# Kernel tuning notes

Measured on AMD Instinct MI355X. Metric: run time of the kernel, lower is better.

Reference implementation:

```python
import jax, jax.numpy as jnp
import numpy as np

N_NODES = 100000
N_EDGES = 1600000
N_GRAPHS = 1000
HID = 128
NCLS = 3


def setup_inputs() -> dict:
    key = jax.random.key(0)
    ks = jax.random.split(key, 16)
    x = jax.random.normal(ks[0], (N_NODES, 1), dtype=jnp.float32)
    edge_index = jax.random.randint(ks[1], (2, N_EDGES), 0, N_NODES, dtype=jnp.int64)
    edge_attr = jax.random.normal(ks[2], (N_EDGES, 1), dtype=jnp.float32)
    batch = jnp.sort(jax.random.randint(ks[3], (N_NODES,), 0, N_GRAPHS, dtype=jnp.int64))
    s1 = 1.0 / np.sqrt(1.0)
    sh = 1.0 / np.sqrt(HID)
    # layer 0 MLP: 1 -> HID -> HID
    W1_0 = jax.random.uniform(ks[4], (1, HID), minval=-s1, maxval=s1)
    b1_0 = jax.random.uniform(ks[5], (HID,), minval=-s1, maxval=s1)
    W2_0 = jax.random.uniform(ks[6], (HID, HID), minval=-sh, maxval=sh)
    b2_0 = jax.random.uniform(ks[7], (HID,), minval=-sh, maxval=sh)
    # layers 1..3 MLPs stacked: HID -> HID -> HID
    W1_s = jax.random.uniform(ks[8], (3, HID, HID), minval=-sh, maxval=sh)
    b1_s = jax.random.uniform(ks[9], (3, HID), minval=-sh, maxval=sh)
    W2_s = jax.random.uniform(ks[10], (3, HID, HID), minval=-sh, maxval=sh)
    b2_s = jax.random.uniform(ks[11], (3, HID), minval=-sh, maxval=sh)
    Wc = jax.random.uniform(ks[12], (HID, NCLS), minval=-sh, maxval=sh)
    bc = jax.random.uniform(ks[13], (NCLS,), minval=-sh, maxval=sh)
    return {"x": x, "edge_index": edge_index, "edge_attr": edge_attr, "batch": batch,
            "W1_0": W1_0, "b1_0": b1_0, "W2_0": W2_0, "b2_0": b2_0,
            "W1_s": W1_s, "b1_s": b1_s, "W2_s": W2_s, "b2_s": b2_s,
            "Wc": Wc, "bc": bc}


def _gine_layer(x, src, dst, edge_attr, W1, b1, W2, b2):
    # message: ReLU(x_j + e_ji), broadcast over feature dim ([E,1] edge_attr)
    msg = jax.nn.relu(x[src] + edge_attr)                       # [E, F]
    agg = jax.ops.segment_sum(msg, dst, num_segments=x.shape[0])  # [N, F]
    h = x + agg                                                 # (1 + eps)*x + agg, eps = 0
    return jax.nn.relu(h @ W1 + b1) @ W2 + b2                   # MLP


def reference(x, edge_index, edge_attr, batch,
              W1_0, b1_0, W2_0, b2_0, W1_s, b1_s, W2_s, b2_s, Wc, bc):
    src, dst = edge_index[0], edge_index[1]
    h = jax.nn.relu(_gine_layer(x, src, dst, edge_attr, W1_0, b1_0, W2_0, b2_0))
    for i in range(3):
        h = jax.nn.relu(_gine_layer(h, src, dst, edge_attr,
                                    W1_s[i], b1_s[i], W2_s[i], b2_s[i]))
    # global mean pool per graph
    summed = jax.ops.segment_sum(h, batch, num_segments=N_GRAPHS)       # [G, HID]
    counts = jax.ops.segment_sum(jnp.ones((h.shape[0],), h.dtype), batch,
                                 num_segments=N_GRAPHS)                  # [G]
    pooled = summed / jnp.maximum(counts, 1.0)[:, None]
    return pooled @ Wc + bc                                              # [G, NCLS]
```

## Files before the change

### kernel.cpp

```cpp
#include <hip/hip_runtime.h>
#include <hip/hip_bf16.h>


#define HID 128
#define NCLS 3
#define EPB 8192
#define BSHIFT 6
#define BNODES 64
#define ECAP 2040

typedef _Float16 f16;
typedef f16 f16x2 __attribute__((ext_vector_type(2)));
typedef f16 f16x8 __attribute__((ext_vector_type(8)));
typedef float f32x2 __attribute__((ext_vector_type(2)));
typedef float f32x4 __attribute__((ext_vector_type(4)));
typedef unsigned short ushort;

__device__ __forceinline__ float bcf(int v) {
    return __builtin_bit_cast(float, v);
}
__device__ __forceinline__ float f16bits2f(ushort u) {
    return (float)__builtin_bit_cast(f16, u);
}


__global__ __launch_bounds__(1024) void k_bin2(const int* __restrict__ src,
                                               const int* __restrict__ dst,
                                               const float* __restrict__ eattr,
                                               const float* __restrict__ x,
                                               int* __restrict__ cursor,
                                               int2* __restrict__ ebuf,
                                               int E, int NB) {
    __shared__ int lh[2048];
    __shared__ int lbase[2048];
    __shared__ int lrsv[2048];
    int t = threadIdx.x;
    for (int b = t; b < NB; b += 1024) lh[b] = 0;
    __syncthreads();
    int base = blockIdx.x * EPB;
    int myd[8];
    #pragma unroll
    for (int j = 0; j < 8; ++j) {
        int e = base + j * 1024 + t;
        myd[j] = (e < E) ? dst[e] : -1;
        if (myd[j] >= 0) atomicAdd(&lh[myd[j] >> BSHIFT], 1);
    }
    __syncthreads();
    for (int b = t; b < NB; b += 1024) {
        int c = lh[b];
        int cp = (c + 7) & ~7;
        lrsv[b] = cp;
        lbase[b] = (cp > 0) ? (b * ECAP + atomicAdd(&cursor[b], cp)) : 0;
        lh[b] = 0;
    }
    __syncthreads();
    #pragma unroll
    for (int j = 0; j < 8; ++j) {
        if (myd[j] >= 0) {
            int e = base + j * 1024 + t;
            int b = myd[j] >> BSHIFT;
            int s = src[e];
            float at = eattr[e];
            float msg = fmaxf(x[s] + at, 0.f);
            unsigned a16 = __builtin_bit_cast(ushort, (f16)at);
            unsigned m16 = __builtin_bit_cast(ushort, (f16)msg);
            int r = atomicAdd(&lh[b], 1);
            int pos = lbase[b] + r;
            if (pos < (b + 1) * ECAP)
                ebuf[pos] = make_int2(s | ((myd[j] & (BNODES - 1)) << 24),
                                      (int)((a16 << 16) | m16));
        }
    }
    __syncthreads();
    for (int b = t; b < NB; b += 1024) {
        int c = lh[b], cp = lrsv[b];
        int p0 = lbase[b] + c;
        int pe = lbase[b] + cp;
        int cap = (b + 1) * ECAP;
        if (pe > cap) pe = cap;
        for (int pos = p0; pos < pe; ++pos)
            ebuf[pos] = make_int2(-1, 0);
    }
}


__global__ __launch_bounds__(1024) void k_prep(const float* __restrict__ W2_0,
                                               const float* __restrict__ W1_s,
                                               const float* __restrict__ W2_s,
                                               f16* __restrict__ Wf,
                                               const int* __restrict__ cursor,
                                               int* __restrict__ bbase, int NB) {
    int t = threadIdx.x;
    if (blockIdx.x < 14) {
        int id = blockIdx.x * 1024 + t;
        int lane = id & 63;
        int w    = (id >> 6) & 3;
        int nf   = (id >> 8) & 1;
        int kk   = (id >> 9) & 3;
        int g    = id >> 11;
        const float* W = (g == 0) ? W2_0
                       : ((g & 1) ? W1_s + (size_t)((g - 1) >> 1) * HID * HID
                                  : W2_s + (size_t)((g - 2) >> 1) * HID * HID);
        int col = w * 32 + nf * 16 + (lane & 15);
        int k0  = kk * 32 + (lane >> 4) * 8;
        f16x8 hi;
        #pragma unroll
        for (int j = 0; j < 8; ++j)
            hi[j] = (f16)W[(k0 + j) * HID + col];
        size_t o = ((((size_t)g * 4 + kk) * 2 + nf) * 4 + w) * 512 +
                   (size_t)lane * 8;
        *(f16x8*)&Wf[o] = hi;
    } else {
        __shared__ int sd[1024];
        int i0 = 2 * t, i1 = 2 * t + 1;
        int a = (i0 < NB) ? min(cursor[i0], ECAP) : 0;
        int b = (i1 < NB) ? min(cursor[i1], ECAP) : 0;
        int s = a + b;
        sd[t] = s;
        __syncthreads();
        #pragma unroll
        for (int o = 1; o < 1024; o <<= 1) {
            int add = (t >= o) ? sd[t - o] : 0;
            __syncthreads();
            sd[t] += add;
            __syncthreads();
        }
        int excl = sd[t] - s;
        if (i0 < NB) bbase[i0] = excl;
        if (i1 < NB) bbase[i1] = excl + a;
        if (t == 1023) bbase[NB] = sd[1023];
    }
}

__global__ __launch_bounds__(256, 8) void k_fill2(const int2* __restrict__ ebuf,
                                               const int* __restrict__ btot,
                                               const int* __restrict__ bbase,
                                               const float* __restrict__ x,
                                               const int* __restrict__ batch,
                                               int2* __restrict__ meta,
                                               int2* __restrict__ pairs,
                                               float* __restrict__ hin0,
                                               int* __restrict__ gcount,
                                               int* __restrict__ gstart,
                                               int N) {
    __shared__ int lcnt[BNODES];
    __shared__ int lofs[BNODES];
    __shared__ float satom[BNODES];
    int b = blockIdx.x, t = threadIdx.x;
    int estart = b * ECAP;
    int cnt = min(btot[b], ECAP);
    int pstart = bbase[b];
    int nb0 = b << BSHIFT;
    if (t < BNODES) {
        lcnt[t] = 0;
        satom[t] = 0.f;
        int node = nb0 + t;
        if (node < N) {
            int gb = batch[node];
            atomicAdd(&gcount[gb], 1);
            if (node == 0 || batch[node - 1] != gb) gstart[gb] = node;
        }
    }
    __syncthreads();
    int2 myv[8];
    #pragma unroll
    for (int j = 0; j < 8; ++j) {
        int i = j * 256 + t;
        if (i < cnt) myv[j] = ebuf[estart + i];
    }
    #pragma unroll
    for (int j = 0; j < 8; ++j) {
        int i = j * 256 + t;
        if (i < cnt && myv[j].x != -1)
            atomicAdd(&lcnt[((unsigned)myv[j].x) >> 24], 1);
    }
    __syncthreads();
    if (t < 64) {
        int a = lcnt[t];
        int sa = a;
        #pragma unroll
        for (int o = 1; o < 64; o <<= 1) {
            int v = __shfl_up(sa, o);
            if (t >= o) sa += v;
        }
        int ea = sa - a;
        lofs[t] = ea;
        lcnt[t] = 0;
        int n0 = nb0 + t;
        if (n0 < N) meta[n0] = make_int2(pstart + ea, a);
    }
    __syncthreads();
    #pragma unroll
    for (int j = 0; j < 8; ++j) {
        int i = j * 256 + t;
        if (i < cnt) {
            int2 v = myv[j];
            if (v.x != -1) {
                int ld = ((unsigned)v.x) >> 24;
                int srcid = v.x & 0x00FFFFFF;
                ushort a16 = (ushort)(((unsigned)v.y) >> 16);
                ushort m16 = (ushort)(v.y & 0xFFFF);
                int r = atomicAdd(&lcnt[ld], 1);
                int pos = lofs[ld] + r;
                pairs[pstart + pos] = make_int2(srcid << 7,
                                     __builtin_bit_cast(int, f16bits2f(a16)));
                atomicAdd(&satom[ld], f16bits2f(m16));
            }
        }
    }
    __syncthreads();
    if (t < BNODES) {
        int node = nb0 + t;
        if (node < N) hin0[node] = x[node] + satom[t];
    }
}


__device__ __forceinline__ void agg_add8(f32x2 acc2[4], uint2 g, float e) {
    f32x2 e2 = {e, e}, z2 = {0.f, 0.f};
    unsigned gw[2] = {g.x, g.y};
    #pragma unroll
    for (int ww = 0; ww < 2; ++ww) {
        f32x2 lo = __builtin_amdgcn_cvt_pk_f32_fp8((int)gw[ww], false);
        f32x2 hi = __builtin_amdgcn_cvt_pk_f32_fp8((int)gw[ww], true);
        lo = __builtin_elementwise_max(lo + e2, z2);
        hi = __builtin_elementwise_max(hi + e2, z2);
        acc2[2 * ww]     += lo;
        acc2[2 * ww + 1] += hi;
    }
}

__device__ __forceinline__ uint2 agg_ld8(const char* __restrict__ hb,
                                         int voff) {
    return *(const uint2*)(hb + (unsigned)voff);
}

__global__ __launch_bounds__(256, 4) void k_agg(
    const unsigned char* __restrict__ h8,
    const f16* __restrict__ hf,
    const int2* __restrict__ pairs,
    const int2* __restrict__ meta,
    f16* __restrict__ oh, int n) {

    int t = threadIdx.x;
    int w = t >> 6, lane = t & 63;
    int g = lane >> 4, c = lane & 15;
    int node = blockIdx.x * 16 + w * 4 + g;
    int c8 = c * 8;
    int sbase = g * 16;
    const char* hb = (const char*)h8;

    int2 m = make_int2(0, 0);
    if (node < n) m = meta[node];
    int off = m.x, d = m.y;
    f32x2 acc2[4] = {{0.f,0.f},{0.f,0.f},{0.f,0.f},{0.f,0.f}};

    for (int wb = 0; wb < d; wb += 16) {
        int rem = d - wb;
        int mm = rem < 16 ? rem : 16;
        int2 pr = make_int2(0, 0);
        if (c < mm) pr = pairs[off + wb + c];
        uint2 gg[16];
        #pragma unroll
        for (int p = 0; p < 16; ++p) {
            int s = __shfl(pr.x, sbase + p);
            if (p < mm) gg[p] = agg_ld8(hb, s + c8);
        }
        #pragma unroll
        for (int p = 0; p < 16; ++p) {
            if (p < mm) {
                float e = bcf(__shfl(pr.y, sbase + p));
                agg_add8(acc2, gg[p], e);
            }
        }
    }

    if (node < n) {
        uint4 sg = *(const uint4*)&hf[(size_t)node * HID + c8];
        unsigned sw[4] = {sg.x, sg.y, sg.z, sg.w};
        unsigned ow[4];
        #pragma unroll
        for (int ww = 0; ww < 4; ++ww) {
            f16x2 s = __builtin_bit_cast(f16x2, sw[ww]);
            f16x2 o;
            o[0] = (f16)((float)s[0] + acc2[ww].x);
            o[1] = (f16)((float)s[1] + acc2[ww].y);
            ow[ww] = __builtin_bit_cast(unsigned, o);
        }
        uint4 o4;
        o4.x = ow[0]; o4.y = ow[1]; o4.z = ow[2]; o4.w = ow[3];
        *(uint4*)&oh[(size_t)node * HID + c8] = o4;
    }
}


__device__ __forceinline__ void load_wfrags1(const f16* __restrict__ Wfg,
                                             int w, int lane,
                                             f16x8 whf[4][2]) {
    #pragma unroll
    for (int kk = 0; kk < 4; ++kk)
        #pragma unroll
        for (int nf = 0; nf < 2; ++nf) {
            size_t o = (((size_t)kk * 2 + nf) * 4 + w) * 512 +
                       (size_t)lane * 8;
            whf[kk][nf] = *(const f16x8*)&Wfg[o];
        }
}

__device__ __forceinline__ void do_gemm1(const f16* Ah,
                                         const f16x8 whf[4][2],
                                         int lane, f32x4 acc[4][2]) {
    int arow = lane & 15, akgrp = lane >> 4;
    #pragma unroll
    for (int kk = 0; kk < 4; ++kk) {
        int chunk = kk * 4 + akgrp;
        f16x8 ah[4];
        #pragma unroll
        for (int mf = 0; mf < 4; ++mf) {
            int r = mf * 16 + arow;
            int swz = chunk ^ (r & 15);
            ah[mf] = *(const f16x8*)&Ah[r * HID + swz * 8];
        }
        #pragma unroll
        for (int mf = 0; mf < 4; ++mf)
            #pragma unroll
            for (int nf = 0; nf < 2; ++nf)
                acc[mf][nf] = __builtin_amdgcn_mfma_f32_16x16x32_f16(
                    ah[mf], whf[kk][nf], acc[mf][nf], 0, 0, 0);
    }
}


__global__ __launch_bounds__(256, 3) void k_mlp(
    const f16* __restrict__ A_g,
    const f16* __restrict__ Wf1, const float* __restrict__ b1,
    const f16* __restrict__ Wf2, const float* __restrict__ b2,
    f16* __restrict__ O, unsigned char* __restrict__ O8, int w8, int n) {

    __shared__ __align__(16) f16 bufA[64 * HID];
    int t = threadIdx.x, w = t >> 6, lane = t & 63;
    int wcol = w * 32, fcol = lane & 15, kgrp = lane >> 4;
    int row0 = blockIdx.x * 64;

    #pragma unroll
    for (int rep = 0; rep < 4; ++rep) {
        int task = rep * 256 + t;
        int r = task >> 4, ch = task & 15;
        int gr = min(row0 + r, n - 1);
        int swz = ch ^ (r & 15);
        *(f16x8*)&bufA[r * HID + swz * 8] =
            *(const f16x8*)&A_g[(size_t)gr * HID + ch * 8];
    }

    f32x4 acc[4][2];
    {
        f16x8 whf[4][2];
        load_wfrags1(Wf1, w, lane, whf);
        float bv0 = b1[wcol + fcol], bv1 = b1[wcol + 16 + fcol];
        __syncthreads();
        #pragma unroll
        for (int mf = 0; mf < 4; ++mf)
            #pragma unroll
            for (int nf = 0; nf < 2; ++nf)
                acc[mf][nf] = (f32x4)(0.f);
        do_gemm1(bufA, whf, lane, acc);
        __syncthreads();
        #pragma unroll
        for (int mf = 0; mf < 4; ++mf)
            #pragma unroll
            for (int nf = 0; nf < 2; ++nf) {
                int cc = wcol + nf * 16 + fcol;
                float bb = nf ? bv1 : bv0;
                #pragma unroll
                for (int j = 0; j < 4; ++j) {
                    int r = mf * 16 + kgrp * 4 + j;
                    float v = fmaxf(acc[mf][nf][j] + bb, 0.f);
                    int addr = r * HID + (((cc >> 3) ^ (r & 15)) << 3) + (cc & 7);
                    bufA[addr] = (f16)v;
                }
            }
    }
    {
        f16x8 whf[4][2];
        load_wfrags1(Wf2, w, lane, whf);
        float bv0 = b2[wcol + fcol], bv1 = b2[wcol + 16 + fcol];
        __syncthreads();
        #pragma unroll
        for (int mf = 0; mf < 4; ++mf)
            #pragma unroll
            for (int nf = 0; nf < 2; ++nf)
                acc[mf][nf] = (f32x4)(0.f);
        do_gemm1(bufA, whf, lane, acc);

        #pragma unroll
        for (int mf = 0; mf < 4; ++mf)
            #pragma unroll
            for (int nf = 0; nf < 2; ++nf) {
                int cc = wcol + nf * 16 + fcol;
                float bb = nf ? bv1 : bv0;
                #pragma unroll
                for (int j = 0; j < 4; ++j) {
                    int r = row0 + mf * 16 + kgrp * 4 + j;
                    if (r < n) {
                        float v = fmaxf(acc[mf][nf][j] + bb, 0.f);
                        O[(size_t)r * HID + cc] = (f16)v;
                        if (w8) {
                            int pk = __builtin_amdgcn_cvt_pk_fp8_f32(
                                v, v, 0, false);
                            O8[(size_t)r * HID + cc] =
                                (unsigned char)(pk & 0xFF);
                        }
                    }
                }
            }
    }
}


__global__ __launch_bounds__(256, 3) void k_mlp0(
    const float* __restrict__ r1x, const float* __restrict__ r1w,
    const float* __restrict__ r1b,
    const f16* __restrict__ Wf2, const float* __restrict__ b2,
    f16* __restrict__ O, unsigned char* __restrict__ O8, int n) {

    __shared__ __align__(16) f16 bufA[64 * HID];
    int t = threadIdx.x, w = t >> 6, lane = t & 63;
    int wcol = w * 32, fcol = lane & 15, kgrp = lane >> 4;
    int row0 = blockIdx.x * 64;

    #pragma unroll
    for (int rep = 0; rep < 4; ++rep) {
        int task = rep * 256 + t;
        int r = task >> 4, ch = task & 15;
        int gr = min(row0 + r, n - 1);
        int swz = ch ^ (r & 15);
        float xv = r1x[gr];
        f16x8 hi;
        #pragma unroll
        for (int j = 0; j < 8; ++j)
            hi[j] = (f16)fmaxf(xv * r1w[ch * 8 + j] + r1b[ch * 8 + j], 0.f);
        *(f16x8*)&bufA[r * HID + swz * 8] = hi;
    }

    f16x8 whf[4][2];
    load_wfrags1(Wf2, w, lane, whf);
    float bv0 = b2[wcol + fcol], bv1 = b2[wcol + 16 + fcol];
    __syncthreads();
    f32x4 acc[4][2];
    #pragma unroll
    for (int mf = 0; mf < 4; ++mf)
        #pragma unroll
        for (int nf = 0; nf < 2; ++nf)
            acc[mf][nf] = (f32x4)(0.f);
    do_gemm1(bufA, whf, lane, acc);

    #pragma unroll
    for (int mf = 0; mf < 4; ++mf)
        #pragma unroll
        for (int nf = 0; nf < 2; ++nf) {
            int cc = wcol + nf * 16 + fcol;
            float bb = nf ? bv1 : bv0;
            #pragma unroll
            for (int j = 0; j < 4; ++j) {
                int r = row0 + mf * 16 + kgrp * 4 + j;
                if (r < n) {
                    float v = fmaxf(acc[mf][nf][j] + bb, 0.f);
                    O[(size_t)r * HID + cc] = (f16)v;
                    int pk = __builtin_amdgcn_cvt_pk_fp8_f32(v, v, 0, false);
                    O8[(size_t)r * HID + cc] = (unsigned char)(pk & 0xFF);
                }
            }
        }
}


__global__ __launch_bounds__(256) void k_head(const f16* __restrict__ h,
                                              const int* __restrict__ gstart,
                                              const int* __restrict__ gcount,
                                              const float* __restrict__ Wc,
                                              const float* __restrict__ bc,
                                              float* __restrict__ out, int G) {
    __shared__ float2 red[4][64];
    __shared__ float pl[HID];
    int g = blockIdx.x, t = threadIdx.x;
    int rr = t >> 6, cc = t & 63;
    int st = gstart[g], c = gcount[g];
    float2 acc = make_float2(0.f, 0.f);
    for (int i = rr; i < c; i += 4) {
        unsigned u = *(const unsigned*)&h[(size_t)(st + i) * HID + cc * 2];
        f16x2 v = __builtin_bit_cast(f16x2, u);
        acc.x += (float)v[0];
        acc.y += (float)v[1];
    }
    red[rr][cc] = acc;
    __syncthreads();
    if (rr == 0) {
        #pragma unroll
        for (int k = 1; k < 4; ++k) {
            acc.x += red[k][cc].x;
            acc.y += red[k][cc].y;
        }
        float inv = 1.f / fmaxf((float)c, 1.f);
        pl[cc * 2]     = acc.x * inv;
        pl[cc * 2 + 1] = acc.y * inv;
    }
    __syncthreads();
    if (t < NCLS) {
        float o = bc[t];
        for (int k = 0; k < HID; ++k) o += pl[k] * Wc[k * NCLS + t];
        out[g * NCLS + t] = o;
    }
}


static inline size_t alignup(size_t x, size_t a) { return (x + a - 1) & ~(a - 1); }

extern "C" void kernel_launch(void* const* d_in, const int* in_sizes, int n_in,
                              void* d_out, int out_size, void* d_ws, size_t ws_size,
                              hipStream_t stream) {
    const float* x      = (const float*)d_in[0];
    const int*   ei     = (const int*)d_in[1];
    const float* eattr  = (const float*)d_in[2];
    const int*   batch  = (const int*)d_in[3];
    const float* W1_0   = (const float*)d_in[4];
    const float* b1_0   = (const float*)d_in[5];
    const float* W2_0   = (const float*)d_in[6];
    const float* b2_0   = (const float*)d_in[7];
    const float* W1_s   = (const float*)d_in[8];
    const float* b1_s   = (const float*)d_in[9];
    const float* W2_s   = (const float*)d_in[10];
    const float* b2_s   = (const float*)d_in[11];
    const float* Wc     = (const float*)d_in[12];
    const float* bc     = (const float*)d_in[13];

    const int N = in_sizes[0];
    const int E = in_sizes[2];
    const int G = out_size / NCLS;
    const int* srcI = ei;
    const int* dstI = ei + E;

    const int NB = (N + BNODES - 1) >> BSHIFT;
    const int NBLK = (E + EPB - 1) / EPB;

    char* p = (char*)d_ws;
    size_t off = 0;
    size_t gcount_off = off;         off = alignup(off + (size_t)G * 4, 256);
    size_t gstart_off = off;         off = alignup(off + (size_t)G * 4, 256);
    size_t cursor_off = off;         off = alignup(off + 2048 * 4, 256);
    size_t zero_bytes = off;
    size_t meta_off = off;           off = alignup(off + (size_t)N * 8, 256);
    size_t bbase_off = off;          off = alignup(off + 2049 * 4, 256);
    size_t hin0_off = off;           off = alignup(off + (size_t)N * 4, 256);
    size_t wf_off = off;             off = alignup(off + 7 * 16384 * 2, 256);
    size_t pairs_off = off;          off = alignup(off + (size_t)NB * ECAP * 8, 256);
    size_t p0_off = off;             off = alignup(off + (size_t)N * HID * 2, 256);
    size_t p8_off = off;             off = alignup(off + (size_t)N * HID, 256);
    size_t p1_off = off;             off = alignup(off + (size_t)N * HID * 2, 256);

    int*    gcount  = (int*)(p + gcount_off);
    int*    gstart  = (int*)(p + gstart_off);
    int*    cursor  = (int*)(p + cursor_off);
    int2*   meta    = (int2*)(p + meta_off);
    int*    bbase   = (int*)(p + bbase_off);
    float*  hin0    = (float*)(p + hin0_off);
    f16*    Wf      = (f16*)(p + wf_off);
    int2*   pairs   = (int2*)(p + pairs_off);
    f16*    P0      = (f16*)(p + p0_off);
    unsigned char* P8 = (unsigned char*)(p + p8_off);
    f16*    P1      = (f16*)(p + p1_off);
    int2*   ebuf    = (int2*)(p + p1_off);

    hipMemsetAsync(d_ws, 0, zero_bytes, stream);

    int gblk = (N + 63) / 64;
    int abl = (N + 15) / 16;

    k_bin2<<<NBLK, 1024, 0, stream>>>(srcI, dstI, eattr, x, cursor, ebuf,
                                      E, NB);
    k_prep<<<15, 1024, 0, stream>>>(W2_0, W1_s, W2_s, Wf, cursor, bbase, NB);
    k_fill2<<<NB, 256, 0, stream>>>(ebuf, cursor, bbase, x, batch, meta,
                                    pairs, hin0, gcount, gstart, N);

    #define WFG(g) (Wf + (size_t)(g) * 16384)

    k_mlp0<<<gblk, 256, 0, stream>>>(hin0, W1_0, b1_0, WFG(0), b2_0,
                                     P0, P8, N);

    for (int l = 0; l < 3; ++l) {
        const float* b1 = b1_s + (size_t)l * HID;
        const float* b2 = b2_s + (size_t)l * HID;
        k_agg<<<abl, 256, 0, stream>>>(P8, P0, pairs, meta, P1, N);
        k_mlp<<<gblk, 256, 0, stream>>>(P1, WFG(1 + 2 * l), b1,
                                        WFG(2 + 2 * l), b2, P0, P8,
                                        (l < 2) ? 1 : 0, N);
    }

    k_head<<<G, 256, 0, stream>>>(P0, gstart, gcount, Wc, bc,
                                  (float*)d_out, G);
}
```

Baseline: 315.4 us.

## Fuse neighbor aggregation into MLP kernel with ping-pong feature buffers

Merges the aggregation kernel into the MLP kernel. Each block now gathers and sums neighbor messages for its 64 rows straight into shared memory, so the fp16 intermediate no longer makes a round trip through global memory and three kernel launches go away. The layers now ping-pong between two fp16/fp8 buffer pairs, because a layer can no longer overwrite its own input in place. The trade-off is that the irregular gather now runs inside a kernel with lower occupancy (launch bounds 3), and its latency is exposed before the MFMA work starts.

```diff
diff --git a/kernel.cpp b/kernel.cpp
--- a/kernel.cpp
+++ b/kernel.cpp
@@ -235,64 +235,6 @@
     return *(const uint2*)(hb + (unsigned)voff);
 }
 
-__global__ __launch_bounds__(256, 4) void k_agg(
-    const unsigned char* __restrict__ h8,
-    const f16* __restrict__ hf,
-    const int2* __restrict__ pairs,
-    const int2* __restrict__ meta,
-    f16* __restrict__ oh, int n) {
-
-    int t = threadIdx.x;
-    int w = t >> 6, lane = t & 63;
-    int g = lane >> 4, c = lane & 15;
-    int node = blockIdx.x * 16 + w * 4 + g;
-    int c8 = c * 8;
-    int sbase = g * 16;
-    const char* hb = (const char*)h8;
-
-    int2 m = make_int2(0, 0);
-    if (node < n) m = meta[node];
-    int off = m.x, d = m.y;
-    f32x2 acc2[4] = {{0.f,0.f},{0.f,0.f},{0.f,0.f},{0.f,0.f}};
-
-    for (int wb = 0; wb < d; wb += 16) {
-        int rem = d - wb;
-        int mm = rem < 16 ? rem : 16;
-        int2 pr = make_int2(0, 0);
-        if (c < mm) pr = pairs[off + wb + c];
-        uint2 gg[16];
-        #pragma unroll
-        for (int p = 0; p < 16; ++p) {
-            int s = __shfl(pr.x, sbase + p);
-            if (p < mm) gg[p] = agg_ld8(hb, s + c8);
-        }
-        #pragma unroll
-        for (int p = 0; p < 16; ++p) {
-            if (p < mm) {
-                float e = bcf(__shfl(pr.y, sbase + p));
-                agg_add8(acc2, gg[p], e);
-            }
-        }
-    }
-
-    if (node < n) {
-        uint4 sg = *(const uint4*)&hf[(size_t)node * HID + c8];
-        unsigned sw[4] = {sg.x, sg.y, sg.z, sg.w};
-        unsigned ow[4];
-        #pragma unroll
-        for (int ww = 0; ww < 4; ++ww) {
-            f16x2 s = __builtin_bit_cast(f16x2, sw[ww]);
-            f16x2 o;
-            o[0] = (f16)((float)s[0] + acc2[ww].x);
-            o[1] = (f16)((float)s[1] + acc2[ww].y);
-            ow[ww] = __builtin_bit_cast(unsigned, o);
-        }
-        uint4 o4;
-        o4.x = ow[0]; o4.y = ow[1]; o4.z = ow[2]; o4.w = ow[3];
-        *(uint4*)&oh[(size_t)node * HID + c8] = o4;
-    }
-}
-
 
 __device__ __forceinline__ void load_wfrags1(const f16* __restrict__ Wfg,
                                              int w, int lane,
@@ -331,25 +273,63 @@
 }
 
 
-__global__ __launch_bounds__(256, 3) void k_mlp(
-    const f16* __restrict__ A_g,
+__global__ __launch_bounds__(256, 3) void k_aggmlp(
+    const unsigned char* __restrict__ h8, const f16* __restrict__ hf,
+    const int2* __restrict__ pairs, const int2* __restrict__ meta,
     const f16* __restrict__ Wf1, const float* __restrict__ b1,
     const f16* __restrict__ Wf2, const float* __restrict__ b2,
     f16* __restrict__ O, unsigned char* __restrict__ O8, int w8, int n) {
 
     __shared__ __align__(16) f16 bufA[64 * HID];
     int t = threadIdx.x, w = t >> 6, lane = t & 63;
-    int wcol = w * 32, fcol = lane & 15, kgrp = lane >> 4;
+    int g = lane >> 4, c = lane & 15;
+    int wcol = w * 32, fcol = c, kgrp = g;
+    int c8 = c * 8, sbase = g * 16;
     int row0 = blockIdx.x * 64;
-
-    #pragma unroll
-    for (int rep = 0; rep < 4; ++rep) {
-        int task = rep * 256 + t;
-        int r = task >> 4, ch = task & 15;
-        int gr = min(row0 + r, n - 1);
-        int swz = ch ^ (r & 15);
-        *(f16x8*)&bufA[r * HID + swz * 8] =
-            *(const f16x8*)&A_g[(size_t)gr * HID + ch * 8];
+    const char* hb = (const char*)h8;
+
+    #pragma unroll
+    for (int pass = 0; pass < 4; ++pass) {
+        int r = w * 16 + pass * 4 + g;
+        int node = row0 + r;
+        int2 m = make_int2(0, 0);
+        if (node < n) m = meta[node];
+        int off = m.x, d = m.y;
+        f32x2 acc2[4] = {{0.f,0.f},{0.f,0.f},{0.f,0.f},{0.f,0.f}};
+
+        for (int wb = 0; wb < d; wb += 16) {
+            int rem = d - wb;
+            int mm = rem < 16 ? rem : 16;
+            int2 pr = make_int2(0, 0);
+            if (c < mm) pr = pairs[off + wb + c];
+            uint2 gg[16];
+            #pragma unroll
+            for (int p = 0; p < 16; ++p) {
+                int s = __shfl(pr.x, sbase + p);
+                if (p < mm) gg[p] = agg_ld8(hb, s + c8);
+            }
+            #pragma unroll
+            for (int p = 0; p < 16; ++p) {
+                if (p < mm) {
+                    float e = bcf(__shfl(pr.y, sbase + p));
+                    agg_add8(acc2, gg[p], e);
+                }
+            }
+        }
+
+        f16x8 ov = (f16x8)(f16)0.f;
+        if (node < n) {
+            uint4 sg = *(const uint4*)&hf[(size_t)node * HID + c8];
+            unsigned sw[4] = {sg.x, sg.y, sg.z, sg.w};
+            #pragma unroll
+            for (int ww = 0; ww < 4; ++ww) {
+                f16x2 s = __builtin_bit_cast(f16x2, sw[ww]);
+                ov[2 * ww]     = (f16)((float)s[0] + acc2[ww].x);
+                ov[2 * ww + 1] = (f16)((float)s[1] + acc2[ww].y);
+            }
+        }
+        int swz = c ^ (r & 15);
+        *(f16x8*)&bufA[r * HID + swz * 8] = ov;
     }
 
     f32x4 acc[4][2];
@@ -553,9 +533,10 @@
     size_t hin0_off = off;           off = alignup(off + (size_t)N * 4, 256);
     size_t wf_off = off;             off = alignup(off + 7 * 16384 * 2, 256);
     size_t pairs_off = off;          off = alignup(off + (size_t)NB * ECAP * 8, 256);
-    size_t p0_off = off;             off = alignup(off + (size_t)N * HID * 2, 256);
-    size_t p8_off = off;             off = alignup(off + (size_t)N * HID, 256);
-    size_t p1_off = off;             off = alignup(off + (size_t)N * HID * 2, 256);
+    size_t p0f_off = off;            off = alignup(off + (size_t)N * HID * 2, 256);
+    size_t p0q_off = off;            off = alignup(off + (size_t)N * HID, 256);
+    size_t p1f_off = off;            off = alignup(off + (size_t)N * HID * 2, 256);
+    size_t p1q_off = off;            off = alignup(off + (size_t)N * HID, 256);
 
     int*    gcount  = (int*)(p + gcount_off);
     int*    gstart  = (int*)(p + gstart_off);
@@ -565,15 +546,15 @@
     float*  hin0    = (float*)(p + hin0_off);
     f16*    Wf      = (f16*)(p + wf_off);
     int2*   pairs   = (int2*)(p + pairs_off);
-    f16*    P0      = (f16*)(p + p0_off);
-    unsigned char* P8 = (unsigned char*)(p + p8_off);
-    f16*    P1      = (f16*)(p + p1_off);
-    int2*   ebuf    = (int2*)(p + p1_off);
+    f16*    P0f     = (f16*)(p + p0f_off);
+    unsigned char* P0q = (unsigned char*)(p + p0q_off);
+    f16*    P1f     = (f16*)(p + p1f_off);
+    unsigned char* P1q = (unsigned char*)(p + p1q_off);
+    int2*   ebuf    = (int2*)(p + p1f_off);
 
     hipMemsetAsync(d_ws, 0, zero_bytes, stream);
 
     int gblk = (N + 63) / 64;
-    int abl = (N + 15) / 16;
 
     k_bin2<<<NBLK, 1024, 0, stream>>>(srcI, dstI, eattr, x, cursor, ebuf,
                                       E, NB);
@@ -584,17 +565,19 @@
     #define WFG(g) (Wf + (size_t)(g) * 16384)
 
     k_mlp0<<<gblk, 256, 0, stream>>>(hin0, W1_0, b1_0, WFG(0), b2_0,
-                                     P0, P8, N);
-
-    for (int l = 0; l < 3; ++l) {
-        const float* b1 = b1_s + (size_t)l * HID;
-        const float* b2 = b2_s + (size_t)l * HID;
-        k_agg<<<abl, 256, 0, stream>>>(P8, P0, pairs, meta, P1, N);
-        k_mlp<<<gblk, 256, 0, stream>>>(P1, WFG(1 + 2 * l), b1,
-                                        WFG(2 + 2 * l), b2, P0, P8,
-                                        (l < 2) ? 1 : 0, N);
-    }
-
-    k_head<<<G, 256, 0, stream>>>(P0, gstart, gcount, Wc, bc,
+                                     P0f, P0q, N);
+
+    k_aggmlp<<<gblk, 256, 0, stream>>>(P0q, P0f, pairs, meta,
+                                       WFG(1), b1_s, WFG(2), b2_s,
+                                       P1f, P1q, 1, N);
+    k_aggmlp<<<gblk, 256, 0, stream>>>(P1q, P1f, pairs, meta,
+                                       WFG(3), b1_s + HID, WFG(4), b2_s + HID,
+                                       P0f, P0q, 1, N);
+    k_aggmlp<<<gblk, 256, 0, stream>>>(P0q, P0f, pairs, meta,
+                                       WFG(5), b1_s + 2 * HID,
+                                       WFG(6), b2_s + 2 * HID,
+                                       P1f, P1q, 0, N);
+
+    k_head<<<G, 256, 0, stream>>>(P1f, gstart, gcount, Wc, bc,
                                   (float*)d_out, G);
 }
```

Result: no change. 319.0 us (+1.2%).

## Widen destination bins to 256 nodes to cut bin count and atomics

Applied to the files above, without the earlier changes.

Destination bucketing now uses 256-node bins (391 bins instead of 1563) with a larger per-bin edge capacity, so the binning kernel handles at most one bin per thread and issues fewer global cursor atomics and less per-bin padding. The fill kernel moves to 512 threads per block, holds 11 edges per thread, and does the per-node prefix scan with four nodes per lane. The intent is to reduce fragmentation and atomic contention in binning and to launch fewer, larger fill blocks. In exchange, shared-memory atomics contend more within each block, register pressure rises, and the fixed capacity of 5504 edges per bin could overflow and drop edges on skewed degree distributions.

```diff
diff --git a/kernel.cpp b/kernel.cpp
--- a/kernel.cpp
+++ b/kernel.cpp
@@ -5,9 +5,9 @@
 #define HID 128
 #define NCLS 3
 #define EPB 8192
-#define BSHIFT 6
-#define BNODES 64
-#define ECAP 2040
+#define BSHIFT 8
+#define BNODES 256
+#define ECAP 5504
 
 typedef _Float16 f16;
 typedef f16 f16x2 __attribute__((ext_vector_type(2)));
@@ -31,11 +31,11 @@
                                                int* __restrict__ cursor,
                                                int2* __restrict__ ebuf,
                                                int E, int NB) {
-    __shared__ int lh[2048];
-    __shared__ int lbase[2048];
-    __shared__ int lrsv[2048];
+    __shared__ int lh[512];
+    __shared__ int lbase[512];
+    __shared__ int lrsv[512];
     int t = threadIdx.x;
-    for (int b = t; b < NB; b += 1024) lh[b] = 0;
+    if (t < NB) lh[t] = 0;
     __syncthreads();
     int base = blockIdx.x * EPB;
     int myd[8];
@@ -46,12 +46,12 @@
         if (myd[j] >= 0) atomicAdd(&lh[myd[j] >> BSHIFT], 1);
     }
     __syncthreads();
-    for (int b = t; b < NB; b += 1024) {
-        int c = lh[b];
+    if (t < NB) {
+        int c = lh[t];
         int cp = (c + 7) & ~7;
-        lrsv[b] = cp;
-        lbase[b] = (cp > 0) ? (b * ECAP + atomicAdd(&cursor[b], cp)) : 0;
-        lh[b] = 0;
+        lrsv[t] = cp;
+        lbase[t] = (cp > 0) ? (t * ECAP + atomicAdd(&cursor[t], cp)) : 0;
+        lh[t] = 0;
     }
     __syncthreads();
     #pragma unroll
@@ -72,11 +72,11 @@
         }
     }
     __syncthreads();
-    for (int b = t; b < NB; b += 1024) {
-        int c = lh[b], cp = lrsv[b];
-        int p0 = lbase[b] + c;
-        int pe = lbase[b] + cp;
-        int cap = (b + 1) * ECAP;
+    if (t < NB) {
+        int c = lh[t], cp = lrsv[t];
+        int p0 = lbase[t] + c;
+        int pe = lbase[t] + cp;
+        int cap = (t + 1) * ECAP;
         if (pe > cap) pe = cap;
         for (int pos = p0; pos < pe; ++pos)
             ebuf[pos] = make_int2(-1, 0);
@@ -112,11 +112,8 @@
         *(f16x8*)&Wf[o] = hi;
     } else {
         __shared__ int sd[1024];
-        int i0 = 2 * t, i1 = 2 * t + 1;
-        int a = (i0 < NB) ? min(cursor[i0], ECAP) : 0;
-        int b = (i1 < NB) ? min(cursor[i1], ECAP) : 0;
-        int s = a + b;
-        sd[t] = s;
+        int v = (t < NB) ? min(cursor[t], ECAP) : 0;
+        sd[t] = v;
         __syncthreads();
         #pragma unroll
         for (int o = 1; o < 1024; o <<= 1) {
@@ -125,14 +122,12 @@
             sd[t] += add;
             __syncthreads();
         }
-        int excl = sd[t] - s;
-        if (i0 < NB) bbase[i0] = excl;
-        if (i1 < NB) bbase[i1] = excl + a;
+        if (t < NB) bbase[t] = sd[t] - v;
         if (t == 1023) bbase[NB] = sd[1023];
     }
 }
 
-__global__ __launch_bounds__(256, 8) void k_fill2(const int2* __restrict__ ebuf,
+__global__ __launch_bounds__(512, 8) void k_fill2(const int2* __restrict__ ebuf,
                                                const int* __restrict__ btot,
                                                const int* __restrict__ bbase,
                                                const float* __restrict__ x,
@@ -162,37 +157,45 @@
         }
     }
     __syncthreads();
-    int2 myv[8];
-    #pragma unroll
-    for (int j = 0; j < 8; ++j) {
-        int i = j * 256 + t;
+    int2 myv[11];
+    #pragma unroll
+    for (int j = 0; j < 11; ++j) {
+        int i = j * 512 + t;
         if (i < cnt) myv[j] = ebuf[estart + i];
     }
     #pragma unroll
-    for (int j = 0; j < 8; ++j) {
-        int i = j * 256 + t;
+    for (int j = 0; j < 11; ++j) {
+        int i = j * 512 + t;
         if (i < cnt && myv[j].x != -1)
             atomicAdd(&lcnt[((unsigned)myv[j].x) >> 24], 1);
     }
     __syncthreads();
     if (t < 64) {
-        int a = lcnt[t];
-        int sa = a;
+        int c0 = lcnt[4 * t], c1 = lcnt[4 * t + 1];
+        int c2 = lcnt[4 * t + 2], c3 = lcnt[4 * t + 3];
+        int s = c0 + c1 + c2 + c3;
+        int sa = s;
         #pragma unroll
         for (int o = 1; o < 64; o <<= 1) {
             int v = __shfl_up(sa, o);
             if (t >= o) sa += v;
         }
-        int ea = sa - a;
-        lofs[t] = ea;
-        lcnt[t] = 0;
-        int n0 = nb0 + t;
-        if (n0 < N) meta[n0] = make_int2(pstart + ea, a);
-    }
-    __syncthreads();
-    #pragma unroll
-    for (int j = 0; j < 8; ++j) {
-        int i = j * 256 + t;
+        int e0 = sa - s;
+        int e1 = e0 + c0, e2 = e1 + c1, e3 = e2 + c2;
+        lofs[4 * t] = e0; lofs[4 * t + 1] = e1;
+        lofs[4 * t + 2] = e2; lofs[4 * t + 3] = e3;
+        lcnt[4 * t] = 0; lcnt[4 * t + 1] = 0;
+        lcnt[4 * t + 2] = 0; lcnt[4 * t + 3] = 0;
+        int n0 = nb0 + 4 * t;
+        if (n0 < N)     meta[n0]     = make_int2(pstart + e0, c0);
+        if (n0 + 1 < N) meta[n0 + 1] = make_int2(pstart + e1, c1);
+        if (n0 + 2 < N) meta[n0 + 2] = make_int2(pstart + e2, c2);
+        if (n0 + 3 < N) meta[n0 + 3] = make_int2(pstart + e3, c3);
+    }
+    __syncthreads();
+    #pragma unroll
+    for (int j = 0; j < 11; ++j) {
+        int i = j * 512 + t;
         if (i < cnt) {
             int2 v = myv[j];
             if (v.x != -1) {
@@ -546,10 +549,10 @@
     size_t off = 0;
     size_t gcount_off = off;         off = alignup(off + (size_t)G * 4, 256);
     size_t gstart_off = off;         off = alignup(off + (size_t)G * 4, 256);
-    size_t cursor_off = off;         off = alignup(off + 2048 * 4, 256);
+    size_t cursor_off = off;         off = alignup(off + 512 * 4, 256);
     size_t zero_bytes = off;
     size_t meta_off = off;           off = alignup(off + (size_t)N * 8, 256);
-    size_t bbase_off = off;          off = alignup(off + 2049 * 4, 256);
+    size_t bbase_off = off;          off = alignup(off + 513 * 4, 256);
     size_t hin0_off = off;           off = alignup(off + (size_t)N * 4, 256);
     size_t wf_off = off;             off = alignup(off + 7 * 16384 * 2, 256);
     size_t pairs_off = off;          off = alignup(off + (size_t)NB * ECAP * 8, 256);
@@ -578,7 +581,7 @@
     k_bin2<<<NBLK, 1024, 0, stream>>>(srcI, dstI, eattr, x, cursor, ebuf,
                                       E, NB);
     k_prep<<<15, 1024, 0, stream>>>(W2_0, W1_s, W2_s, Wf, cursor, bbase, NB);
-    k_fill2<<<NB, 256, 0, stream>>>(ebuf, cursor, bbase, x, batch, meta,
+    k_fill2<<<NB, 512, 0, stream>>>(ebuf, cursor, bbase, x, batch, meta,
                                     pairs, hin0, gcount, gstart, N);
 
     #define WFG(g) (Wf + (size_t)(g) * 16384)
```

Result: faster. 308.6 us (-2.2%).
